# Kernel optimization log

Hardware: AMD Instinct MI355X
Metric: run time of the kernel (lower is better)

Reference implementation:

```python
import jax, jax.numpy as jnp
import numpy as np

B, S, D, E = 8, 2048, 1024, 8


def setup_inputs() -> dict:
    key = jax.random.key(0)
    k1, k2, k3, k4 = jax.random.split(key, 4)
    return {
        "x": jax.random.normal(k1, (B, S, D), dtype=jnp.float32),
        "routing_scores": jax.random.normal(k2, (B, E), dtype=jnp.float32),
        "expert_w": jax.random.normal(k3, (E, D, D), dtype=jnp.float32) / np.sqrt(D),
        "expert_b": jax.random.normal(k4, (E, D), dtype=jnp.float32),
        "k": 2,
    }


def reference(x, routing_scores, expert_w, expert_b, k):
    batch = routing_scores.shape[0]
    # top-k gating mask + renormalization scale (torch.topk + scatter_ equivalent)
    values, indices = jax.lax.top_k(routing_scores, k)              # (B, k)
    mask = jnp.zeros_like(routing_scores, dtype=bool)
    mask = mask.at[jnp.arange(batch)[:, None], indices].set(True)    # (B, E)
    scale = 1.0 / (values.sum(axis=1, keepdims=True) + 1e-8)         # (B, 1)
    masked_scores = scale * routing_scores * mask                    # (B, E)

    # dense per-expert transform: expert_e(x) = x @ W_e + b_e  -> (E, B, S, D)
    expert_out = jnp.einsum("bsd,edf->ebsf", x, expert_w) + expert_b[:, None, None, :]
    # weighted scatter-accumulate over experts (zero weight for inactive pairs)
    final_output = jnp.einsum("be,ebsf->bsf", masked_scores, expert_out)

    return final_output, mask.sum(axis=0)
```

## Files before the change

### kernel.cpp

```cpp
#include <hip/hip_runtime.h>

#define NB 8
#define NS 2048
#define ND 1024
#define NE 8

typedef unsigned short ushort_t;
typedef __attribute__((ext_vector_type(8))) short bf16x8;
typedef __attribute__((ext_vector_type(4))) float f32x4;

__device__ __forceinline__ unsigned short f2bf(float f) {
    union { float f; unsigned int u; } x; x.f = f;
    unsigned int u = x.u + 0x7fffu + ((x.u >> 16) & 1u);
    return (unsigned short)(u >> 16);
}

__device__ __forceinline__ void gload16(const void* g, void* l) {
    __builtin_amdgcn_global_load_lds(
        (const __attribute__((address_space(1))) unsigned int*)g,
        (__attribute__((address_space(3))) unsigned int*)l, 16, 0, 0);
}

__global__ void routing_kernel(const float* __restrict__ scores,
                               const int* __restrict__ kp,
                               float* __restrict__ coef,
                               float* __restrict__ counts) {
    __shared__ int selS[NB][NE];
    int t = threadIdx.x;
    int k = *kp;
    if (t < NB) {
        float s[NE];
#pragma unroll
        for (int e = 0; e < NE; ++e) s[e] = scores[t * NE + e];
        bool sel[NE];
#pragma unroll
        for (int e = 0; e < NE; ++e) sel[e] = false;
        float sum = 0.f;
        for (int j = 0; j < k; ++j) {
            int best = 0; float bv = -3.4e38f;
#pragma unroll
            for (int e = 0; e < NE; ++e)
                if (!sel[e] && s[e] > bv) { bv = s[e]; best = e; }
            sel[best] = true; sum += bv;
        }
        float scale = 1.f / (sum + 1e-8f);
#pragma unroll
        for (int e = 0; e < NE; ++e) {
            coef[t * NE + e] = sel[e] ? scale * s[e] : 0.f;
            selS[t][e] = sel[e] ? 1 : 0;
        }
    }
    __syncthreads();
    if (t < NE) {
        int c = 0;
#pragma unroll
        for (int b = 0; b < NB; ++b) c += selS[b][t];
        counts[t] = (float)c;
    }
}

__global__ void bias_kernel(const float* __restrict__ eb,
                            const float* __restrict__ coef,
                            float* __restrict__ bias) {
    int b = blockIdx.y;
    int f = blockIdx.x * 256 + threadIdx.x;
    float acc = 0.f;
#pragma unroll
    for (int e = 0; e < NE; ++e) {
        float c = coef[b * NE + e];
        if (c != 0.f) acc += c * eb[e * ND + f];
    }
    bias[b * ND + f] = acc;
}

__global__ void combine_kernel(const float* __restrict__ W,
                               const float* __restrict__ coef,
                               ushort_t* __restrict__ wct) {
    __shared__ float tile[64][65];
    int b = blockIdx.z;
    int d0 = blockIdx.y * 64, f0 = blockIdx.x * 64;
    int t = threadIdx.x;
    int lr = t >> 4;
    int lc = (t & 15) * 4;
    float4 acc[4];
#pragma unroll
    for (int it = 0; it < 4; ++it) acc[it] = make_float4(0.f, 0.f, 0.f, 0.f);
#pragma unroll
    for (int e = 0; e < NE; ++e) {
        float c = coef[b * NE + e];
        if (c != 0.f) {
            const float* We = W + ((size_t)e * ND * ND);
#pragma unroll
            for (int it = 0; it < 4; ++it) {
                int d = d0 + lr + it * 16;
                float4 v = *(const float4*)(We + (size_t)d * ND + f0 + lc);
                acc[it].x += c * v.x; acc[it].y += c * v.y;
                acc[it].z += c * v.z; acc[it].w += c * v.w;
            }
        }
    }
#pragma unroll
    for (int it = 0; it < 4; ++it) {
        int r = lr + it * 16;
        tile[r][lc + 0] = acc[it].x; tile[r][lc + 1] = acc[it].y;
        tile[r][lc + 2] = acc[it].z; tile[r][lc + 3] = acc[it].w;
    }
    __syncthreads();
    int dl = t & 63;
    int frow = t >> 6;
    ushort_t* dst = wct + (size_t)b * ND * ND + (size_t)f0 * ND + d0 + dl;
#pragma unroll
    for (int it = 0; it < 16; ++it) {
        int f = frow + it * 4;
        dst[(size_t)f * ND] = f2bf(tile[dl][f]);
    }
}

__global__ void convert_kernel(const float* __restrict__ x, ushort_t* __restrict__ xb) {
    int i = blockIdx.x * 256 + threadIdx.x;
    const float4* p = (const float4*)x + 2 * (size_t)i;
    float4 a = p[0], b = p[1];
    uint4 o;
    o.x = (unsigned)f2bf(a.x) | ((unsigned)f2bf(a.y) << 16);
    o.y = (unsigned)f2bf(a.z) | ((unsigned)f2bf(a.w) << 16);
    o.z = (unsigned)f2bf(b.x) | ((unsigned)f2bf(b.y) << 16);
    o.w = (unsigned)f2bf(b.z) | ((unsigned)f2bf(b.w) << 16);
    ((uint4*)xb)[i] = o;
}

__global__ __launch_bounds__(512, 2) void gemm_kernel(const ushort_t* __restrict__ xb,
                                                      const ushort_t* __restrict__ wct,
                                                      const float* __restrict__ bias,
                                                      float* __restrict__ out) {
    __shared__ ushort_t ldsA[2][256 * 64];
    __shared__ ushort_t ldsB[2][256 * 64];

    int bid = blockIdx.x;
    int b = bid & 7;
    int tile = bid >> 3;
    int m0 = (tile >> 2) * 256;
    int n0 = (tile & 3) * 256;
    const ushort_t* A  = xb  + ((size_t)b * NS * ND) + (size_t)m0 * ND;
    const ushort_t* Bt = wct + ((size_t)b * ND * ND) + (size_t)n0 * ND;

    int t = threadIdx.x, lane = t & 63, wave = t >> 6;
    int wm = wave >> 2, wn = wave & 3;
    int fr = lane & 15, fq = lane >> 4;

    int srow = lane >> 3;
    int sslot = (lane & 7) ^ srow;
    const ushort_t* gA[4];
    const ushort_t* gB[4];
#pragma unroll
    for (int i = 0; i < 4; ++i) {
        int r = (i * 8 + wave) * 8 + srow;
        gA[i] = A  + (size_t)r * ND + sslot * 8;
        gB[i] = Bt + (size_t)r * ND + sslot * 8;
    }

    int sA = fq ^ (fr & 7);
    int aoff[8], boff[4];
#pragma unroll
    for (int mi = 0; mi < 8; ++mi) aoff[mi] = (wm * 128 + mi * 16 + fr) * 128 + sA * 16;
#pragma unroll
    for (int nj = 0; nj < 4; ++nj) boff[nj] = (wn * 64 + nj * 16 + fr) * 128 + sA * 16;

    f32x4 acc[8][4];
#pragma unroll
    for (int i = 0; i < 8; ++i)
#pragma unroll
        for (int j = 0; j < 4; ++j) acc[i][j] = (f32x4){0.f, 0.f, 0.f, 0.f};

#pragma unroll
    for (int i = 0; i < 4; ++i) {
        gload16(gA[i], (char*)&ldsA[0][0] + (i * 8 + wave) * 1024);
        gload16(gB[i], (char*)&ldsB[0][0] + (i * 8 + wave) * 1024);
        gA[i] += 64; gB[i] += 64;
    }
    asm volatile("s_waitcnt vmcnt(0)" ::: "memory");
    __builtin_amdgcn_s_barrier();

    const int NT = ND / 64;
    for (int kt = 0; kt < NT; ++kt) {
        int cb = kt & 1;
        bool pre = (kt + 1 < NT);
        const char* lA = (const char*)&ldsA[cb][0];
        const char* lB = (const char*)&ldsB[cb][0];
        char* dA = (char*)&ldsA[cb ^ 1][0];
        char* dB = (char*)&ldsB[cb ^ 1][0];

        bf16x8 af[4], bfr[4];

#pragma unroll
        for (int nj = 0; nj < 4; ++nj) bfr[nj] = *(const bf16x8*)(lB + boff[nj]);
#pragma unroll
        for (int mi = 0; mi < 4; ++mi) af[mi] = *(const bf16x8*)(lA + aoff[mi]);
        if (pre) {
#pragma unroll
            for (int i = 0; i < 4; ++i) {
                gload16(gA[i], dA + (i * 8 + wave) * 1024);
                gA[i] += 64;
            }
        }
        __builtin_amdgcn_sched_barrier(0);
        __builtin_amdgcn_s_barrier();
        asm volatile("s_waitcnt lgkmcnt(0)" ::: "memory");
        __builtin_amdgcn_sched_barrier(0);
        __builtin_amdgcn_s_setprio(1);
#pragma unroll
        for (int mi = 0; mi < 4; ++mi)
#pragma unroll
            for (int nj = 0; nj < 4; ++nj)
                acc[mi][nj] = __builtin_amdgcn_mfma_f32_16x16x32_bf16(af[mi], bfr[nj], acc[mi][nj], 0, 0, 0);
        __builtin_amdgcn_s_setprio(0);
        __builtin_amdgcn_s_barrier();

#pragma unroll
        for (int mi = 0; mi < 4; ++mi) af[mi] = *(const bf16x8*)(lA + aoff[mi + 4]);
        if (pre) {
#pragma unroll
            for (int i = 0; i < 4; ++i) {
                gload16(gB[i], dB + (i * 8 + wave) * 1024);
                gB[i] += 64;
            }
        }
        __builtin_amdgcn_sched_barrier(0);
        __builtin_amdgcn_s_barrier();
        asm volatile("s_waitcnt lgkmcnt(0)" ::: "memory");
        __builtin_amdgcn_sched_barrier(0);
        __builtin_amdgcn_s_setprio(1);
#pragma unroll
        for (int mi = 0; mi < 4; ++mi)
#pragma unroll
            for (int nj = 0; nj < 4; ++nj)
                acc[mi + 4][nj] = __builtin_amdgcn_mfma_f32_16x16x32_bf16(af[mi], bfr[nj], acc[mi + 4][nj], 0, 0, 0);
        __builtin_amdgcn_s_setprio(0);
        __builtin_amdgcn_s_barrier();

#pragma unroll
        for (int nj = 0; nj < 4; ++nj) bfr[nj] = *(const bf16x8*)(lB + (boff[nj] ^ 64));
#pragma unroll
        for (int mi = 0; mi < 4; ++mi) af[mi] = *(const bf16x8*)(lA + (aoff[mi] ^ 64));
        __builtin_amdgcn_sched_barrier(0);
        __builtin_amdgcn_s_barrier();
        asm volatile("s_waitcnt lgkmcnt(0)" ::: "memory");
        __builtin_amdgcn_sched_barrier(0);
        __builtin_amdgcn_s_setprio(1);
#pragma unroll
        for (int mi = 0; mi < 4; ++mi)
#pragma unroll
            for (int nj = 0; nj < 4; ++nj)
                acc[mi][nj] = __builtin_amdgcn_mfma_f32_16x16x32_bf16(af[mi], bfr[nj], acc[mi][nj], 0, 0, 0);
        __builtin_amdgcn_s_setprio(0);
        __builtin_amdgcn_s_barrier();

#pragma unroll
        for (int mi = 0; mi < 4; ++mi) af[mi] = *(const bf16x8*)(lA + (aoff[mi + 4] ^ 64));
        __builtin_amdgcn_sched_barrier(0);
        __builtin_amdgcn_s_barrier();
        asm volatile("s_waitcnt lgkmcnt(0)" ::: "memory");
        __builtin_amdgcn_sched_barrier(0);
        __builtin_amdgcn_s_setprio(1);
#pragma unroll
        for (int mi = 0; mi < 4; ++mi)
#pragma unroll
            for (int nj = 0; nj < 4; ++nj)
                acc[mi + 4][nj] = __builtin_amdgcn_mfma_f32_16x16x32_bf16(af[mi], bfr[nj], acc[mi + 4][nj], 0, 0, 0);
        __builtin_amdgcn_s_setprio(0);
        asm volatile("s_waitcnt vmcnt(0)" ::: "memory");
        __builtin_amdgcn_s_barrier();
    }

    const float* bs = bias + b * ND;
    float* O = out + ((size_t)b * NS * ND);
#pragma unroll
    for (int mi = 0; mi < 8; ++mi) {
        int row = m0 + wm * 128 + mi * 16 + fq * 4;
#pragma unroll
        for (int nj = 0; nj < 4; ++nj) {
            int col = n0 + wn * 64 + nj * 16 + fr;
            float bv = bs[col];
            f32x4 v = acc[mi][nj];
#pragma unroll
            for (int r = 0; r < 4; ++r)
                O[(size_t)(row + r) * ND + col] = v[r] + bv;
        }
    }
}

extern "C" void kernel_launch(void* const* d_in, const int* in_sizes, int n_in,
                              void* d_out, int out_size, void* d_ws, size_t ws_size,
                              hipStream_t stream) {
    const float* x      = (const float*)d_in[0];
    const float* scores = (const float*)d_in[1];
    const float* Wx     = (const float*)d_in[2];
    const float* eb     = (const float*)d_in[3];
    const int*   kp     = (const int*)d_in[4];
    float* out = (float*)d_out;
    char* ws = (char*)d_ws;

    float*    coef  = (float*)(ws);
    float*    bias  = (float*)(ws + 1024);
    ushort_t* xbuf  = (ushort_t*)(ws + 65536);
    ushort_t* wct   = (ushort_t*)(ws + 65536 + (size_t)NB * NS * ND * 2);
    float*    counts = out + (size_t)NB * NS * ND;

    routing_kernel<<<1, 64, 0, stream>>>(scores, kp, coef, counts);
    bias_kernel<<<dim3(ND / 256, NB), 256, 0, stream>>>(eb, coef, bias);
    combine_kernel<<<dim3(ND / 64, ND / 64, NB), 256, 0, stream>>>(Wx, coef, wct);
    convert_kernel<<<dim3(NB * NS * ND / 8 / 256), 256, 0, stream>>>(x, xbuf);
    gemm_kernel<<<256, 512, 0, stream>>>(xbuf, wct, bias, out);
}
```

Baseline: 78.99 us.

## Switch GEMM to 4-stage K=32 LDS pipeline with deeper prefetch

The GEMM main loop now stages K-tiles of 32 in four LDS buffers instead of two buffers of 64. It keeps three tiles in flight using partial vmcnt waits, so global load latency is hidden across more iterations. The LDS row layout and XOR swizzle are rebuilt for the 64-byte rows. In exchange there are twice as many loop iterations and barriers per K, and each iteration does less MFMA work to cover the synchronisation.

Result: no change. 78.55 us (-0.5%).

```diff
diff --git a/kernel.cpp b/kernel.cpp
--- a/kernel.cpp
+++ b/kernel.cpp
@@ -132,8 +132,8 @@
                                                       const ushort_t* __restrict__ wct,
                                                       const float* __restrict__ bias,
                                                       float* __restrict__ out) {
-    __shared__ ushort_t ldsA[2][256 * 64];
-    __shared__ ushort_t ldsB[2][256 * 64];
+    __shared__ ushort_t ldsA[4][256 * 32];
+    __shared__ ushort_t ldsB[4][256 * 32];
 
     int bid = blockIdx.x;
     int b = bid & 7;
@@ -147,23 +147,24 @@
     int wm = wave >> 2, wn = wave & 3;
     int fr = lane & 15, fq = lane >> 4;
 
-    int srow = lane >> 3;
-    int sslot = (lane & 7) ^ srow;
-    const ushort_t* gA[4];
-    const ushort_t* gB[4];
-#pragma unroll
-    for (int i = 0; i < 4; ++i) {
-        int r = (i * 8 + wave) * 8 + srow;
-        gA[i] = A  + (size_t)r * ND + sslot * 8;
-        gB[i] = Bt + (size_t)r * ND + sslot * 8;
-    }
-
-    int sA = fq ^ (fr & 7);
+    int srow = t >> 2;
+    int fsrc = ((t >> 2) & 3) ^ ((t >> 4) & 3);
+    int sslot = (t & 3) ^ fsrc;
+    const ushort_t* gA[2];
+    const ushort_t* gB[2];
+#pragma unroll
+    for (int i = 0; i < 2; ++i) {
+        gA[i] = A  + (size_t)(i * 128 + srow) * ND + sslot * 8;
+        gB[i] = Bt + (size_t)(i * 128 + srow) * ND + sslot * 8;
+    }
+
+    int fswz = (fr & 3) ^ ((fr >> 2) & 3);
+    int slotr = (fq ^ fswz) * 16;
     int aoff[8], boff[4];
 #pragma unroll
-    for (int mi = 0; mi < 8; ++mi) aoff[mi] = (wm * 128 + mi * 16 + fr) * 128 + sA * 16;
-#pragma unroll
-    for (int nj = 0; nj < 4; ++nj) boff[nj] = (wn * 64 + nj * 16 + fr) * 128 + sA * 16;
+    for (int mi = 0; mi < 8; ++mi) aoff[mi] = (wm * 128 + mi * 16 + fr) * 64 + slotr;
+#pragma unroll
+    for (int nj = 0; nj < 4; ++nj) boff[nj] = (wn * 64 + nj * 16 + fr) * 64 + slotr;
 
     f32x4 acc[8][4];
 #pragma unroll
@@ -171,23 +172,32 @@
 #pragma unroll
         for (int j = 0; j < 4; ++j) acc[i][j] = (f32x4){0.f, 0.f, 0.f, 0.f};
 
-#pragma unroll
-    for (int i = 0; i < 4; ++i) {
-        gload16(gA[i], (char*)&ldsA[0][0] + (i * 8 + wave) * 1024);
-        gload16(gB[i], (char*)&ldsB[0][0] + (i * 8 + wave) * 1024);
-        gA[i] += 64; gB[i] += 64;
-    }
-    asm volatile("s_waitcnt vmcnt(0)" ::: "memory");
+    const int NT = ND / 32;
+
+#pragma unroll
+    for (int T = 0; T < 3; ++T) {
+#pragma unroll
+        for (int i = 0; i < 2; ++i) {
+            gload16(gA[i], (char*)&ldsA[T][0] + i * 8192 + wave * 1024);
+            gA[i] += 32;
+        }
+#pragma unroll
+        for (int i = 0; i < 2; ++i) {
+            gload16(gB[i], (char*)&ldsB[T][0] + i * 8192 + wave * 1024);
+            gB[i] += 32;
+        }
+    }
+    asm volatile("s_waitcnt vmcnt(8)" ::: "memory");
     __builtin_amdgcn_s_barrier();
 
-    const int NT = ND / 64;
     for (int kt = 0; kt < NT; ++kt) {
-        int cb = kt & 1;
-        bool pre = (kt + 1 < NT);
-        const char* lA = (const char*)&ldsA[cb][0];
-        const char* lB = (const char*)&ldsB[cb][0];
-        char* dA = (char*)&ldsA[cb ^ 1][0];
-        char* dB = (char*)&ldsB[cb ^ 1][0];
+        int cur = kt & 3;
+        const char* lA = (const char*)&ldsA[cur][0];
+        const char* lB = (const char*)&ldsB[cur][0];
+        bool pre = (kt + 3 < NT);
+        int nb = (kt + 3) & 3;
+        char* dA = (char*)&ldsA[nb][0];
+        char* dB = (char*)&ldsB[nb][0];
 
         bf16x8 af[4], bfr[4];
 
@@ -197,9 +207,9 @@
         for (int mi = 0; mi < 4; ++mi) af[mi] = *(const bf16x8*)(lA + aoff[mi]);
         if (pre) {
 #pragma unroll
-            for (int i = 0; i < 4; ++i) {
-                gload16(gA[i], dA + (i * 8 + wave) * 1024);
-                gA[i] += 64;
+            for (int i = 0; i < 2; ++i) {
+                gload16(gA[i], dA + i * 8192 + wave * 1024);
+                gA[i] += 32;
             }
         }
         __builtin_amdgcn_sched_barrier(0);
@@ -219,9 +229,9 @@
         for (int mi = 0; mi < 4; ++mi) af[mi] = *(const bf16x8*)(lA + aoff[mi + 4]);
         if (pre) {
 #pragma unroll
-            for (int i = 0; i < 4; ++i) {
-                gload16(gB[i], dB + (i * 8 + wave) * 1024);
-                gB[i] += 64;
+            for (int i = 0; i < 2; ++i) {
+                gload16(gB[i], dB + i * 8192 + wave * 1024);
+                gB[i] += 32;
             }
         }
         __builtin_amdgcn_sched_barrier(0);
@@ -235,39 +245,13 @@
             for (int nj = 0; nj < 4; ++nj)
                 acc[mi + 4][nj] = __builtin_amdgcn_mfma_f32_16x16x32_bf16(af[mi], bfr[nj], acc[mi + 4][nj], 0, 0, 0);
         __builtin_amdgcn_s_setprio(0);
-        __builtin_amdgcn_s_barrier();
-
-#pragma unroll
-        for (int nj = 0; nj < 4; ++nj) bfr[nj] = *(const bf16x8*)(lB + (boff[nj] ^ 64));
-#pragma unroll
-        for (int mi = 0; mi < 4; ++mi) af[mi] = *(const bf16x8*)(lA + (aoff[mi] ^ 64));
-        __builtin_amdgcn_sched_barrier(0);
-        __builtin_amdgcn_s_barrier();
-        asm volatile("s_waitcnt lgkmcnt(0)" ::: "memory");
-        __builtin_amdgcn_sched_barrier(0);
-        __builtin_amdgcn_s_setprio(1);
-#pragma unroll
-        for (int mi = 0; mi < 4; ++mi)
-#pragma unroll
-            for (int nj = 0; nj < 4; ++nj)
-                acc[mi][nj] = __builtin_amdgcn_mfma_f32_16x16x32_bf16(af[mi], bfr[nj], acc[mi][nj], 0, 0, 0);
-        __builtin_amdgcn_s_setprio(0);
-        __builtin_amdgcn_s_barrier();
-
-#pragma unroll
-        for (int mi = 0; mi < 4; ++mi) af[mi] = *(const bf16x8*)(lA + (aoff[mi + 4] ^ 64));
-        __builtin_amdgcn_sched_barrier(0);
-        __builtin_amdgcn_s_barrier();
-        asm volatile("s_waitcnt lgkmcnt(0)" ::: "memory");
-        __builtin_amdgcn_sched_barrier(0);
-        __builtin_amdgcn_s_setprio(1);
-#pragma unroll
-        for (int mi = 0; mi < 4; ++mi)
-#pragma unroll
-            for (int nj = 0; nj < 4; ++nj)
-                acc[mi + 4][nj] = __builtin_amdgcn_mfma_f32_16x16x32_bf16(af[mi], bfr[nj], acc[mi + 4][nj], 0, 0, 0);
-        __builtin_amdgcn_s_setprio(0);
-        asm volatile("s_waitcnt vmcnt(0)" ::: "memory");
+        if (kt < NT - 3) {
+            asm volatile("s_waitcnt vmcnt(8)" ::: "memory");
+        } else if (kt == NT - 3) {
+            asm volatile("s_waitcnt vmcnt(4)" ::: "memory");
+        } else if (kt == NT - 2) {
+            asm volatile("s_waitcnt vmcnt(0)" ::: "memory");
+        }
         __builtin_amdgcn_s_barrier();
     }
 
```

## Drop intra-iteration barriers and pipeline LDS fragment loads with partial lgkmcnt waits

Applied to the files above, without the earlier changes.

Rebuilds the GEMM inner k-loop schedule. Before, each k-step used repeated s_barrier plus full lgkmcnt(0) waits between its four MFMA phases. Now most fragments are issued up front into separate register sets, and each MFMA phase waits only for the fragments it needs via partial lgkmcnt counts. A single barrier per iteration remains, after the global-to-LDS prefetch completes. This should cut synchronisation stalls and overlap LDS reads with MFMA, at the cost of more live VGPRs for fragments, which could lower occupancy or cause spills.

Measured after the change: 73.84 us. 1.07x faster.

```diff
diff --git a/kernel.cpp b/kernel.cpp
--- a/kernel.cpp
+++ b/kernel.cpp
@@ -158,43 +158,51 @@
         gB[i] = Bt + (size_t)r * ND + sslot * 8;
     }
 
-    int sA = fq ^ (fr & 7);
+    int slotr = (fq ^ (fr & 7)) * 16;
     int aoff[8], boff[4];
 #pragma unroll
-    for (int mi = 0; mi < 8; ++mi) aoff[mi] = (wm * 128 + mi * 16 + fr) * 128 + sA * 16;
-#pragma unroll
-    for (int nj = 0; nj < 4; ++nj) boff[nj] = (wn * 64 + nj * 16 + fr) * 128 + sA * 16;
+    for (int mi = 0; mi < 8; ++mi) aoff[mi] = (wm * 128 + mi * 16 + fr) * 128 + slotr;
+#pragma unroll
+    for (int nj = 0; nj < 4; ++nj) boff[nj] = (wn * 64 + nj * 16 + fr) * 128 + slotr;
 
     f32x4 acc[8][4];
 #pragma unroll
     for (int i = 0; i < 8; ++i)
 #pragma unroll
         for (int j = 0; j < 4; ++j) acc[i][j] = (f32x4){0.f, 0.f, 0.f, 0.f};
+
+    const int NT = ND / 64;
 
 #pragma unroll
     for (int i = 0; i < 4; ++i) {
         gload16(gA[i], (char*)&ldsA[0][0] + (i * 8 + wave) * 1024);
+        gA[i] += 64;
+    }
+#pragma unroll
+    for (int i = 0; i < 4; ++i) {
         gload16(gB[i], (char*)&ldsB[0][0] + (i * 8 + wave) * 1024);
-        gA[i] += 64; gB[i] += 64;
+        gB[i] += 64;
     }
     asm volatile("s_waitcnt vmcnt(0)" ::: "memory");
     __builtin_amdgcn_s_barrier();
 
-    const int NT = ND / 64;
     for (int kt = 0; kt < NT; ++kt) {
-        int cb = kt & 1;
+        const char* lA = (const char*)&ldsA[kt & 1][0];
+        const char* lB = (const char*)&ldsB[kt & 1][0];
         bool pre = (kt + 1 < NT);
-        const char* lA = (const char*)&ldsA[cb][0];
-        const char* lB = (const char*)&ldsB[cb][0];
-        char* dA = (char*)&ldsA[cb ^ 1][0];
-        char* dB = (char*)&ldsB[cb ^ 1][0];
-
-        bf16x8 af[4], bfr[4];
-
-#pragma unroll
-        for (int nj = 0; nj < 4; ++nj) bfr[nj] = *(const bf16x8*)(lB + boff[nj]);
-#pragma unroll
-        for (int mi = 0; mi < 4; ++mi) af[mi] = *(const bf16x8*)(lA + aoff[mi]);
+        char* dA = (char*)&ldsA[(kt + 1) & 1][0];
+        char* dB = (char*)&ldsB[(kt + 1) & 1][0];
+
+        __builtin_amdgcn_sched_barrier(0);
+        bf16x8 bf0[4], bf1[4], a0[4], a1[4], a2[4], a3[4];
+#pragma unroll
+        for (int nj = 0; nj < 4; ++nj) bf0[nj] = *(const bf16x8*)(lB + boff[nj]);
+#pragma unroll
+        for (int mi = 0; mi < 4; ++mi) a0[mi] = *(const bf16x8*)(lA + aoff[mi]);
+#pragma unroll
+        for (int nj = 0; nj < 4; ++nj) bf1[nj] = *(const bf16x8*)(lB + (boff[nj] ^ 64));
+#pragma unroll
+        for (int mi = 0; mi < 4; ++mi) a1[mi] = *(const bf16x8*)(lA + aoff[mi + 4]);
         if (pre) {
 #pragma unroll
             for (int i = 0; i < 4; ++i) {
@@ -203,20 +211,17 @@
             }
         }
         __builtin_amdgcn_sched_barrier(0);
-        __builtin_amdgcn_s_barrier();
-        asm volatile("s_waitcnt lgkmcnt(0)" ::: "memory");
+        asm volatile("s_waitcnt lgkmcnt(8)" ::: "memory");
         __builtin_amdgcn_sched_barrier(0);
         __builtin_amdgcn_s_setprio(1);
 #pragma unroll
         for (int mi = 0; mi < 4; ++mi)
 #pragma unroll
             for (int nj = 0; nj < 4; ++nj)
-                acc[mi][nj] = __builtin_amdgcn_mfma_f32_16x16x32_bf16(af[mi], bfr[nj], acc[mi][nj], 0, 0, 0);
+                acc[mi][nj] = __builtin_amdgcn_mfma_f32_16x16x32_bf16(a0[mi], bf0[nj], acc[mi][nj], 0, 0, 0);
         __builtin_amdgcn_s_setprio(0);
-        __builtin_amdgcn_s_barrier();
-
-#pragma unroll
-        for (int mi = 0; mi < 4; ++mi) af[mi] = *(const bf16x8*)(lA + aoff[mi + 4]);
+#pragma unroll
+        for (int mi = 0; mi < 4; ++mi) a2[mi] = *(const bf16x8*)(lA + (aoff[mi] ^ 64));
         if (pre) {
 #pragma unroll
             for (int i = 0; i < 4; ++i) {
@@ -225,7 +230,28 @@
             }
         }
         __builtin_amdgcn_sched_barrier(0);
-        __builtin_amdgcn_s_barrier();
+        asm volatile("s_waitcnt lgkmcnt(4)" ::: "memory");
+        __builtin_amdgcn_sched_barrier(0);
+        __builtin_amdgcn_s_setprio(1);
+#pragma unroll
+        for (int mi = 0; mi < 4; ++mi)
+#pragma unroll
+            for (int nj = 0; nj < 4; ++nj)
+                acc[mi + 4][nj] = __builtin_amdgcn_mfma_f32_16x16x32_bf16(a1[mi], bf0[nj], acc[mi + 4][nj], 0, 0, 0);
+        __builtin_amdgcn_s_setprio(0);
+#pragma unroll
+        for (int mi = 0; mi < 4; ++mi) a3[mi] = *(const bf16x8*)(lA + (aoff[mi + 4] ^ 64));
+        __builtin_amdgcn_sched_barrier(0);
+        asm volatile("s_waitcnt lgkmcnt(4)" ::: "memory");
+        __builtin_amdgcn_sched_barrier(0);
+        __builtin_amdgcn_s_setprio(1);
+#pragma unroll
+        for (int mi = 0; mi < 4; ++mi)
+#pragma unroll
+            for (int nj = 0; nj < 4; ++nj)
+                acc[mi][nj] = __builtin_amdgcn_mfma_f32_16x16x32_bf16(a2[mi], bf1[nj], acc[mi][nj], 0, 0, 0);
+        __builtin_amdgcn_s_setprio(0);
+        __builtin_amdgcn_sched_barrier(0);
         asm volatile("s_waitcnt lgkmcnt(0)" ::: "memory");
         __builtin_amdgcn_sched_barrier(0);
         __builtin_amdgcn_s_setprio(1);
@@ -233,42 +259,13 @@
         for (int mi = 0; mi < 4; ++mi)
 #pragma unroll
             for (int nj = 0; nj < 4; ++nj)
-                acc[mi + 4][nj] = __builtin_amdgcn_mfma_f32_16x16x32_bf16(af[mi], bfr[nj], acc[mi + 4][nj], 0, 0, 0);
+                acc[mi + 4][nj] = __builtin_amdgcn_mfma_f32_16x16x32_bf16(a3[mi], bf1[nj], acc[mi + 4][nj], 0, 0, 0);
         __builtin_amdgcn_s_setprio(0);
-        __builtin_amdgcn_s_barrier();
-
-#pragma unroll
-        for (int nj = 0; nj < 4; ++nj) bfr[nj] = *(const bf16x8*)(lB + (boff[nj] ^ 64));
-#pragma unroll
-        for (int mi = 0; mi < 4; ++mi) af[mi] = *(const bf16x8*)(lA + (aoff[mi] ^ 64));
-        __builtin_amdgcn_sched_barrier(0);
-        __builtin_amdgcn_s_barrier();
-        asm volatile("s_waitcnt lgkmcnt(0)" ::: "memory");
-        __builtin_amdgcn_sched_barrier(0);
-        __builtin_amdgcn_s_setprio(1);
-#pragma unroll
-        for (int mi = 0; mi < 4; ++mi)
-#pragma unroll
-            for (int nj = 0; nj < 4; ++nj)
-                acc[mi][nj] = __builtin_amdgcn_mfma_f32_16x16x32_bf16(af[mi], bfr[nj], acc[mi][nj], 0, 0, 0);
-        __builtin_amdgcn_s_setprio(0);
-        __builtin_amdgcn_s_barrier();
-
-#pragma unroll
-        for (int mi = 0; mi < 4; ++mi) af[mi] = *(const bf16x8*)(lA + (aoff[mi + 4] ^ 64));
-        __builtin_amdgcn_sched_barrier(0);
-        __builtin_amdgcn_s_barrier();
-        asm volatile("s_waitcnt lgkmcnt(0)" ::: "memory");
-        __builtin_amdgcn_sched_barrier(0);
-        __builtin_amdgcn_s_setprio(1);
-#pragma unroll
-        for (int mi = 0; mi < 4; ++mi)
-#pragma unroll
-            for (int nj = 0; nj < 4; ++nj)
-                acc[mi + 4][nj] = __builtin_amdgcn_mfma_f32_16x16x32_bf16(af[mi], bfr[nj], acc[mi + 4][nj], 0, 0, 0);
-        __builtin_amdgcn_s_setprio(0);
-        asm volatile("s_waitcnt vmcnt(0)" ::: "memory");
-        __builtin_amdgcn_s_barrier();
+        __builtin_amdgcn_sched_barrier(0);
+        if (pre) {
+            asm volatile("s_waitcnt vmcnt(0)" ::: "memory");
+            __builtin_amdgcn_s_barrier();
+        }
     }
 
     const float* bs = bias + b * ND;
```
